# Performance work log

Hardware: AMD Instinct MI355X
Metric: run time of the kernel (lower is better)

The kernel has to match this reference:

```python
import jax, jax.numpy as jnp
import numpy as np

B, T, HID = 1, 2048, 2048
H = 16            # num_heads == num_key_value_heads
D = HID // H      # head_dim == feature_dim == 128
EPS = 1e-5


def _layer_norm(x, eps=1e-5):
    mu = jnp.mean(x, axis=-1, keepdims=True)
    var = jnp.mean((x - mu) ** 2, axis=-1, keepdims=True)
    return (x - mu) * jax.lax.rsqrt(var + eps)


def _feature_map(x, gamma, beta):
    # ReBased feature map, flatten=False (parallel mode): affine then LayerNorm
    return _layer_norm(x * gamma + beta)


def setup_inputs() -> dict:
    key = jax.random.key(0)
    ks = jax.random.split(key, 8)
    s = HID ** -0.5
    return {
        "hidden_states": jax.random.normal(ks[0], (B, T, HID), jnp.float32),
        "Wq": jax.random.normal(ks[1], (HID, HID), jnp.float32) * s,
        "Wk": jax.random.normal(ks[2], (HID, HID), jnp.float32) * s,
        "Wv": jax.random.normal(ks[3], (HID, HID), jnp.float32) * s,
        "Wo": jax.random.normal(ks[4], (HID, HID), jnp.float32) * s,
        "gamma": 1.0 + 0.1 * jax.random.normal(ks[5], (D,), jnp.float32),
        "beta": 0.1 * jax.random.normal(ks[6], (D,), jnp.float32),
    }


def reference(hidden_states, Wq, Wk, Wv, Wo, gamma, beta):
    b, t, _ = hidden_states.shape
    # projections (nn.Linear: x @ W.T), split into heads: [b, t, h, d]
    q = (hidden_states @ Wq.T).reshape(b, t, H, D)
    k = (hidden_states @ Wk.T).reshape(b, t, H, D)
    v = (hidden_states @ Wv.T).reshape(b, t, H, D)
    # ReBased feature map (no quadratic flatten in parallel mode)
    q = _feature_map(q, gamma, beta)
    k = _feature_map(k, gamma, beta)
    # parallel_rebased: scale q, quadratic score, causal mask, normalize
    q = q * (D ** -0.5)
    attn = jnp.einsum('bqhd,bkhd->bhqk', q, k) ** 2  # (q.k)^2
    mask = jnp.tril(jnp.ones((t, t), dtype=bool))
    attn = jnp.where(mask, attn, 0.0)
    o = jnp.einsum('bhqk,bkhd->bqhd', attn, v)       # [b, t, h, d]
    z = jnp.sum(attn, axis=-1)                       # [b, h, t]
    o = o / (jnp.swapaxes(z, 1, 2)[..., None] + EPS)
    o = o.reshape(b, t, H * D)
    return o @ Wo.T
```

## Files before the change

### kernel.cpp

```cpp
#include <hip/hip_runtime.h>
#include <hip/hip_bf16.h>
#include <stdint.h>

typedef __bf16 bf16;
typedef __bf16 v8bf __attribute__((ext_vector_type(8)));
typedef float  v4f  __attribute__((ext_vector_type(4)));

#define TSEQ   2048
#define HIDDIM 2048
#define NHEAD  16
#define HDIM   128

__device__ __forceinline__ void async16(void* lds, const void* g)
{
    __builtin_amdgcn_global_load_lds(
        (__attribute__((address_space(1))) void*)(uintptr_t)g,
        (__attribute__((address_space(3))) void*)(unsigned int)(uintptr_t)lds,
        16, 0, 0);
}

__global__ __launch_bounds__(256) void conv5(const float* __restrict__ s0, bf16* __restrict__ d0,
                                             const float* __restrict__ s1, bf16* __restrict__ d1,
                                             const float* __restrict__ s2, bf16* __restrict__ d2,
                                             const float* __restrict__ s3, bf16* __restrict__ d3,
                                             const float* __restrict__ s4, bf16* __restrict__ d4)
{
    const float* src; bf16* dst;
    switch (blockIdx.y) {
        case 0: src = s0; dst = d0; break;
        case 1: src = s1; dst = d1; break;
        case 2: src = s2; dst = d2; break;
        case 3: src = s3; dst = d3; break;
        default: src = s4; dst = d4; break;
    }
    const size_t i = ((size_t)blockIdx.x * 256 + threadIdx.x) * 8;
    const float4 a = *(const float4*)(src + i);
    const float4 b = *(const float4*)(src + i + 4);
    v8bf o;
    o[0] = (bf16)a.x; o[1] = (bf16)a.y; o[2] = (bf16)a.z; o[3] = (bf16)a.w;
    o[4] = (bf16)b.x; o[5] = (bf16)b.y; o[6] = (bf16)b.z; o[7] = (bf16)b.w;
    *(v8bf*)(dst + i) = o;
}

template <typename CT>
__device__ __forceinline__ void gemm_body(const bf16* __restrict__ A,
                                          const bf16* __restrict__ B,
                                          CT* __restrict__ C,
                                          int m0, int n0, int K, int ldc)
{
    __shared__ __attribute__((aligned(16))) bf16 sA[128*32];
    __shared__ __attribute__((aligned(16))) bf16 sB[128*32];
    const int tid  = threadIdx.x;
    const int lane = tid & 63;
    const int w    = tid >> 6;
    const int wm   = w >> 1, wn = w & 1;
    const int quad = lane >> 4, lr = lane & 15;
    const int srow = lane >> 2;
    const int scol = (lane & 3) * 8;

    const bf16* gA0 = A + (size_t)(m0 + w*32 + srow) * K + scol;
    const bf16* gB0 = B + (size_t)(n0 + w*32 + srow) * K + scol;
    bf16* lA0 = &sA[w*1024];
    bf16* lB0 = &sB[w*1024];

    v4f acc[4][4] = {};

    for (int kt = 0; kt < K; kt += 32) {
        __syncthreads();
        async16(lA0,       gA0 + kt);
        async16(lA0 + 512, gA0 + (size_t)16*K + kt);
        async16(lB0,       gB0 + kt);
        async16(lB0 + 512, gB0 + (size_t)16*K + kt);
        __syncthreads();
        v8bf a[4], b[4];
#pragma unroll
        for (int i = 0; i < 4; ++i)
            a[i] = *(const v8bf*)&sA[(wm*64 + i*16 + lr)*32 + quad*8];
#pragma unroll
        for (int j = 0; j < 4; ++j)
            b[j] = *(const v8bf*)&sB[(wn*64 + j*16 + lr)*32 + quad*8];
#pragma unroll
        for (int i = 0; i < 4; ++i)
#pragma unroll
            for (int j = 0; j < 4; ++j)
                acc[i][j] = __builtin_amdgcn_mfma_f32_16x16x32_bf16(a[i], b[j], acc[i][j], 0, 0, 0);
    }

#pragma unroll
    for (int i = 0; i < 4; ++i) {
        const int row_b = m0 + wm*64 + i*16 + quad*4;
#pragma unroll
        for (int j = 0; j < 4; ++j) {
            const int col = n0 + wn*64 + j*16 + lr;
#pragma unroll
            for (int r = 0; r < 4; ++r)
                C[(size_t)(row_b + r)*ldc + col] = (CT)acc[i][j][r];
        }
    }
}

__global__ __launch_bounds__(256) void gemm_qkv(const bf16* __restrict__ A,
    const bf16* __restrict__ Wq, const bf16* __restrict__ Wk, const bf16* __restrict__ Wv,
    bf16* __restrict__ qb, bf16* __restrict__ kb, bf16* __restrict__ vb)
{
    const int which = blockIdx.x >> 4;
    const int n0 = (blockIdx.x & 15) * 128;
    const int m0 = blockIdx.y * 128;
    const bf16* B = (which == 0) ? Wq : (which == 1) ? Wk : Wv;
    bf16* C = (which == 0) ? qb : (which == 1) ? kb : vb;
    gemm_body<bf16>(A, B, C, m0, n0, HIDDIM, HIDDIM);
}

__global__ __launch_bounds__(256) void gemm_out(const bf16* __restrict__ A,
    const bf16* __restrict__ B, float* __restrict__ C)
{
    __shared__ __attribute__((aligned(16))) bf16 sA[128*32];
    __shared__ __attribute__((aligned(16))) bf16 sB[64*32];
    const int m0 = blockIdx.y * 128, n0 = blockIdx.x * 64;
    const int K = HIDDIM, ldc = HIDDIM;
    const int tid  = threadIdx.x;
    const int lane = tid & 63;
    const int w    = tid >> 6;
    const int wm   = w >> 1, wn = w & 1;
    const int quad = lane >> 4, lr = lane & 15;
    const int srow = lane >> 2;
    const int scol = (lane & 3) * 8;

    const bf16* gA0 = A + (size_t)(m0 + w*32 + srow) * K + scol;
    const bf16* gB0 = B + (size_t)(n0 + w*16 + srow) * K + scol;
    bf16* lA0 = &sA[w*1024];
    bf16* lB0 = &sB[w*512];

    v4f acc[4][2] = {};

    for (int kt = 0; kt < K; kt += 32) {
        __syncthreads();
        async16(lA0,       gA0 + kt);
        async16(lA0 + 512, gA0 + (size_t)16*K + kt);
        async16(lB0,       gB0 + kt);
        __syncthreads();
        v8bf a[4], b[2];
#pragma unroll
        for (int i = 0; i < 4; ++i)
            a[i] = *(const v8bf*)&sA[(wm*64 + i*16 + lr)*32 + quad*8];
#pragma unroll
        for (int j = 0; j < 2; ++j)
            b[j] = *(const v8bf*)&sB[(wn*32 + j*16 + lr)*32 + quad*8];
#pragma unroll
        for (int i = 0; i < 4; ++i)
#pragma unroll
            for (int j = 0; j < 2; ++j)
                acc[i][j] = __builtin_amdgcn_mfma_f32_16x16x32_bf16(a[i], b[j], acc[i][j], 0, 0, 0);
    }

#pragma unroll
    for (int i = 0; i < 4; ++i) {
        const int row_b = m0 + wm*64 + i*16 + quad*4;
#pragma unroll
        for (int j = 0; j < 2; ++j) {
            const int col = n0 + wn*32 + j*16 + lr;
#pragma unroll
            for (int r = 0; r < 4; ++r)
                C[(size_t)(row_b + r)*ldc + col] = acc[i][j][r];
        }
    }
}

__global__ __launch_bounds__(256) void fmap(bf16* __restrict__ qb, bf16* __restrict__ kb,
                                            const float* __restrict__ gamma,
                                            const float* __restrict__ beta)
{
    const int rid  = blockIdx.x * 4 + (threadIdx.x >> 6);
    const int lane = threadIdx.x & 63;
    bf16* base = (rid < TSEQ*NHEAD) ? (qb + (size_t)rid * HDIM)
                                    : (kb + (size_t)(rid - TSEQ*NHEAD) * HDIM);
    const float scale = (rid < TSEQ*NHEAD) ? 0.08838834764831845f : 1.0f;

    const bf16 x0b = base[lane*2], x1b = base[lane*2+1];
    const float g0 = gamma[lane*2], g1 = gamma[lane*2+1];
    const float b0 = beta[lane*2],  b1 = beta[lane*2+1];
    float x0 = (float)x0b*g0 + b0;
    float x1 = (float)x1b*g1 + b1;
    float s  = x0 + x1;
    float sq = x0*x0 + x1*x1;
#pragma unroll
    for (int off = 1; off < 64; off <<= 1) { s += __shfl_xor(s, off); sq += __shfl_xor(sq, off); }
    const float mu   = s * (1.0f/128.0f);
    float var        = sq * (1.0f/128.0f) - mu*mu;
    var = fmaxf(var, 0.0f);
    const float rstd = rsqrtf(var + 1e-5f);
    base[lane*2]   = (bf16)((x0 - mu) * rstd * scale);
    base[lane*2+1] = (bf16)((x1 - mu) * rstd * scale);
}

__global__ __launch_bounds__(256) void transpose2048(const bf16* __restrict__ src,
                                                     bf16* __restrict__ dst)
{
    __shared__ __attribute__((aligned(16))) bf16 tile[64][72];
    const int t0 = blockIdx.y * 64, c0 = blockIdx.x * 64;
    const int tid = threadIdx.x;
    const int r = tid >> 3;
    const int c = (tid & 7) * 8;
#pragma unroll
    for (int p = 0; p < 2; ++p) {
        const int rr = r + p*32;
        *(v8bf*)&tile[rr][c] = *(const v8bf*)(src + (size_t)(t0+rr)*HIDDIM + c0 + c);
    }
    __syncthreads();
#pragma unroll
    for (int p = 0; p < 2; ++p) {
        const int orow = r + p*32;
        v8bf o;
#pragma unroll
        for (int i = 0; i < 8; ++i) o[i] = tile[c + i][orow];
        *(v8bf*)(dst + (size_t)(c0+orow)*HIDDIM + t0 + c) = o;
    }
}

__global__ __launch_bounds__(256) void attn(const bf16* __restrict__ qb,
                                            const bf16* __restrict__ kb,
                                            const bf16* __restrict__ vt,
                                            bf16* __restrict__ ob)
{
    __shared__ __attribute__((aligned(16))) bf16 sK[64*136];
    __shared__ __attribute__((aligned(16))) bf16 sV[128*72];
    __shared__ __attribute__((aligned(16))) bf16 sS[64*72];
    const int h    = blockIdx.y;
    const int tile = 31 - blockIdx.x;
    const int tid  = threadIdx.x, lane = tid & 63, w = tid >> 6;
    const int quad = lane >> 4, lr = lane & 15;

    v8bf qa[4];
    {
        const bf16* q0 = qb + (size_t)(tile*64 + w*16 + lr)*HIDDIM + h*HDIM + quad*8;
#pragma unroll
        for (int ks = 0; ks < 4; ++ks)
            qa[ks] = *(const v8bf*)(q0 + ks*32);
    }

    const int rK = tid >> 4, cK = (tid & 15) * 8;
    const int rV = tid >> 3, cV = (tid & 7) * 8;

    v8bf curK[4], curV[4], nxtK[4], nxtV[4];
#pragma unroll
    for (int p = 0; p < 4; ++p) {
        curK[p] = *(const v8bf*)(kb + (size_t)(rK + p*16)*HIDDIM + h*HDIM + cK);
        curV[p] = *(const v8bf*)(vt + (size_t)(h*HDIM + rV + p*32)*HIDDIM + cV);
    }

    v4f  o[8] = {};
    float z[4] = {};
    const int nch = tile + 1;

    for (int ch = 0; ch < nch; ++ch) {
        const int s0 = ch * 64;
        const bool diag = (ch == tile);
        __syncthreads();
#pragma unroll
        for (int p = 0; p < 4; ++p)
            *(v8bf*)&sK[(rK + p*16)*136 + cK] = curK[p];
#pragma unroll
        for (int p = 0; p < 4; ++p)
            *(v8bf*)&sV[(rV + p*32)*72 + cV] = curV[p];
        if (ch + 1 < nch) {
            const int s1 = s0 + 64;
#pragma unroll
            for (int p = 0; p < 4; ++p) {
                nxtK[p] = *(const v8bf*)(kb + (size_t)(s1 + rK + p*16)*HIDDIM + h*HDIM + cK);
                nxtV[p] = *(const v8bf*)(vt + (size_t)(h*HDIM + rV + p*32)*HIDDIM + s1 + cV);
            }
        }
        __syncthreads();

        v8bf kbf[4][4];
#pragma unroll
        for (int nj = 0; nj < 4; ++nj)
#pragma unroll
            for (int ks = 0; ks < 4; ++ks)
                kbf[nj][ks] = *(const v8bf*)&sK[(nj*16 + lr)*136 + ks*32 + quad*8];
        const int row_l = w*16 + quad*4;
        const int qg    = tile*64 + row_l;
#pragma unroll
        for (int nj = 0; nj < 4; ++nj) {
            v4f s4 = {0.f, 0.f, 0.f, 0.f};
#pragma unroll
            for (int ks = 0; ks < 4; ++ks)
                s4 = __builtin_amdgcn_mfma_f32_16x16x32_bf16(qa[ks], kbf[nj][ks], s4, 0, 0, 0);
            const int col = nj*16 + lr;
            const int sg  = s0 + col;
#pragma unroll
            for (int r = 0; r < 4; ++r) {
                float val = s4[r] * s4[r];
                if (diag && (sg > qg + r)) val = 0.0f;
                const bf16 vb16 = (bf16)val;
                z[r] += (float)vb16;
                sS[(row_l + r)*72 + col] = vb16;
            }
        }

#pragma unroll
        for (int ks = 0; ks < 2; ++ks) {
            const v8bf sa = *(const v8bf*)&sS[(w*16 + lr)*72 + ks*32 + quad*8];
#pragma unroll
            for (int nd = 0; nd < 8; ++nd) {
                const v8bf vbf = *(const v8bf*)&sV[(nd*16 + lr)*72 + ks*32 + quad*8];
                o[nd] = __builtin_amdgcn_mfma_f32_16x16x32_bf16(sa, vbf, o[nd], 0, 0, 0);
            }
        }

        if (ch + 1 < nch) {
#pragma unroll
            for (int p = 0; p < 4; ++p) { curK[p] = nxtK[p]; curV[p] = nxtV[p]; }
        }
    }

#pragma unroll
    for (int r = 0; r < 4; ++r) {
        float zz = z[r];
        zz += __shfl_xor(zz, 1); zz += __shfl_xor(zz, 2);
        zz += __shfl_xor(zz, 4); zz += __shfl_xor(zz, 8);
        z[r] = zz + 1e-5f;
    }

    {
        const int row_l = w*16 + quad*4;
        const size_t rbase = (size_t)(tile*64 + row_l)*HIDDIM + h*HDIM;
#pragma unroll
        for (int nd = 0; nd < 8; ++nd) {
            const int col = nd*16 + lr;
#pragma unroll
            for (int r = 0; r < 4; ++r)
                ob[rbase + (size_t)r*HIDDIM + col] = (bf16)(o[nd][r] / z[r]);
        }
    }
}

extern "C" void kernel_launch(void* const* d_in, const int* in_sizes, int n_in,
                              void* d_out, int out_size, void* d_ws, size_t ws_size,
                              hipStream_t stream)
{
    const float* hs    = (const float*)d_in[0];
    const float* Wq    = (const float*)d_in[1];
    const float* Wk    = (const float*)d_in[2];
    const float* Wv    = (const float*)d_in[3];
    const float* Wo    = (const float*)d_in[4];
    const float* gamma = (const float*)d_in[5];
    const float* beta  = (const float*)d_in[6];
    float* outp = (float*)d_out;

    const size_t MAT = (size_t)TSEQ * HIDDIM;

    bf16* ws   = (bf16*)d_ws;
    bf16* hs_b = ws + 0*MAT;
    bf16* vt   = hs_b;
    bf16* Wv_b = ws + 1*MAT;
    bf16* Wo_b = ws + 2*MAT;
    bf16* qb   = ws + 3*MAT;
    bf16* kb   = ws + 4*MAT;
    bf16* vb   = ws + 5*MAT;
    bf16* ob   = vb;
    bf16* Wq_b = (bf16*)d_out;
    bf16* Wk_b = (bf16*)d_out + MAT;

    conv5<<<dim3(2048, 5), 256, 0, stream>>>(hs, hs_b, Wq, Wq_b, Wk, Wk_b, Wv, Wv_b, Wo, Wo_b);
    gemm_qkv<<<dim3(48, 16), 256, 0, stream>>>(hs_b, Wq_b, Wk_b, Wv_b, qb, kb, vb);
    fmap<<<dim3(2*TSEQ*NHEAD/4), 256, 0, stream>>>(qb, kb, gamma, beta);
    transpose2048<<<dim3(32, 32), 256, 0, stream>>>(vb, vt);
    attn<<<dim3(32, 16), 256, 0, stream>>>(qb, kb, vt, ob);
    gemm_out<<<dim3(32, 16), 256, 0, stream>>>(ob, Wo_b, outp);
}
```

Before: 299.5 us.

## Pair causal tiles per block and split KV chunks across two wave groups

The attention kernel now launches 16x16 blocks of 512 threads. Each block handles two complementary query tiles (31-pr and pr) so the causal work per block is balanced. Within a block, two groups of four waves each process alternate 64-key chunks into separate LDS buffers, and the partial O and Z accumulators are reduced through shared memory at the end. This targets load imbalance from the causal triangle and the tail, at the cost of much more LDS per block (around 140KB, which limits occupancy) and an extra reduction step.

```diff
diff --git a/kernel.cpp b/kernel.cpp
--- a/kernel.cpp
+++ b/kernel.cpp
@@ -217,120 +217,156 @@
     }
 }
 
-__global__ __launch_bounds__(256) void attn(const bf16* __restrict__ qb,
-                                            const bf16* __restrict__ kb,
-                                            const bf16* __restrict__ vt,
-                                            bf16* __restrict__ ob)
-{
-    __shared__ __attribute__((aligned(16))) bf16 sK[64*136];
-    __shared__ __attribute__((aligned(16))) bf16 sV[128*72];
-    __shared__ __attribute__((aligned(16))) bf16 sS[64*72];
+__global__ __launch_bounds__(512, 2) void attn(const bf16* __restrict__ qb,
+                                               const bf16* __restrict__ kb,
+                                               const bf16* __restrict__ vt,
+                                               bf16* __restrict__ ob)
+{
+    __shared__ __attribute__((aligned(16))) bf16 sK[2*64*136];
+    __shared__ __attribute__((aligned(16))) bf16 sV[2*128*72];
+    __shared__ __attribute__((aligned(16))) bf16 sS[2*64*72];
+    __shared__ __attribute__((aligned(16))) float sO[64*129];
+    __shared__ __attribute__((aligned(16))) float sZ[64*17];
+
     const int h    = blockIdx.y;
-    const int tile = 31 - blockIdx.x;
-    const int tid  = threadIdx.x, lane = tid & 63, w = tid >> 6;
+    const int pr   = blockIdx.x;
+    const int tid  = threadIdx.x, lane = tid & 63;
+    const int w    = tid >> 6;
+    const int g    = w >> 2;
+    const int ww   = w & 3;
     const int quad = lane >> 4, lr = lane & 15;
-
-    v8bf qa[4];
-    {
-        const bf16* q0 = qb + (size_t)(tile*64 + w*16 + lr)*HIDDIM + h*HDIM + quad*8;
-#pragma unroll
-        for (int ks = 0; ks < 4; ++ks)
-            qa[ks] = *(const v8bf*)(q0 + ks*32);
-    }
-
-    const int rK = tid >> 4, cK = (tid & 15) * 8;
-    const int rV = tid >> 3, cV = (tid & 7) * 8;
-
-    v8bf curK[4], curV[4], nxtK[4], nxtV[4];
-#pragma unroll
-    for (int p = 0; p < 4; ++p) {
-        curK[p] = *(const v8bf*)(kb + (size_t)(rK + p*16)*HIDDIM + h*HDIM + cK);
-        curV[p] = *(const v8bf*)(vt + (size_t)(h*HDIM + rV + p*32)*HIDDIM + cV);
-    }
-
-    v4f  o[8] = {};
-    float z[4] = {};
-    const int nch = tile + 1;
-
-    for (int ch = 0; ch < nch; ++ch) {
-        const int s0 = ch * 64;
-        const bool diag = (ch == tile);
-        __syncthreads();
-#pragma unroll
-        for (int p = 0; p < 4; ++p)
-            *(v8bf*)&sK[(rK + p*16)*136 + cK] = curK[p];
-#pragma unroll
-        for (int p = 0; p < 4; ++p)
-            *(v8bf*)&sV[(rV + p*32)*72 + cV] = curV[p];
-        if (ch + 1 < nch) {
-            const int s1 = s0 + 64;
+    const int rs   = tid >> 4;
+    const int cs   = (tid & 15) * 8;
+
+#pragma unroll
+    for (int ti = 0; ti < 2; ++ti) {
+        const int tile = ti ? pr : (31 - pr);
+        const int nch  = tile + 1;
+
+        v8bf qa[4];
+        {
+            const bf16* q0 = qb + (size_t)(tile*64 + ww*16 + lr)*HIDDIM + h*HDIM + quad*8;
+#pragma unroll
+            for (int ks = 0; ks < 4; ++ks)
+                qa[ks] = *(const v8bf*)(q0 + ks*32);
+        }
+
+        v4f  o[8] = {};
+        float z[4] = {0.f, 0.f, 0.f, 0.f};
+
+        v8bf curK[4], curV[4], nxtK[4], nxtV[4];
+#pragma unroll
+        for (int p = 0; p < 4; ++p) {
+            curK[p] = *(const v8bf*)(kb + (size_t)(rs + p*32)*HIDDIM + h*HDIM + cs);
+            curV[p] = *(const v8bf*)(vt + (size_t)(h*HDIM + rs + p*32)*HIDDIM + cs);
+        }
+
+        for (int ich = 0; ich < nch; ich += 2) {
+            __syncthreads();
 #pragma unroll
             for (int p = 0; p < 4; ++p) {
-                nxtK[p] = *(const v8bf*)(kb + (size_t)(s1 + rK + p*16)*HIDDIM + h*HDIM + cK);
-                nxtV[p] = *(const v8bf*)(vt + (size_t)(h*HDIM + rV + p*32)*HIDDIM + s1 + cV);
-            }
-        }
-        __syncthreads();
-
-        v8bf kbf[4][4];
-#pragma unroll
-        for (int nj = 0; nj < 4; ++nj)
-#pragma unroll
-            for (int ks = 0; ks < 4; ++ks)
-                kbf[nj][ks] = *(const v8bf*)&sK[(nj*16 + lr)*136 + ks*32 + quad*8];
-        const int row_l = w*16 + quad*4;
-        const int qg    = tile*64 + row_l;
-#pragma unroll
-        for (int nj = 0; nj < 4; ++nj) {
-            v4f s4 = {0.f, 0.f, 0.f, 0.f};
-#pragma unroll
-            for (int ks = 0; ks < 4; ++ks)
-                s4 = __builtin_amdgcn_mfma_f32_16x16x32_bf16(qa[ks], kbf[nj][ks], s4, 0, 0, 0);
-            const int col = nj*16 + lr;
-            const int sg  = s0 + col;
+                const int r = rs + p*32;
+                *(v8bf*)&sK[(r>>6)*8704 + (r&63)*136 + cs] = curK[p];
+            }
+#pragma unroll
+            for (int p = 0; p < 4; ++p)
+                *(v8bf*)&sV[(cs>>6)*9216 + (rs + p*32)*72 + (cs & 63)] = curV[p];
+
+            if (ich + 2 < nch) {
+                const int s1 = (ich + 2) * 64;
+#pragma unroll
+                for (int p = 0; p < 4; ++p) {
+                    nxtK[p] = *(const v8bf*)(kb + (size_t)(s1 + rs + p*32)*HIDDIM + h*HDIM + cs);
+                    nxtV[p] = *(const v8bf*)(vt + (size_t)(h*HDIM + rs + p*32)*HIDDIM + s1 + cs);
+                }
+            }
+            __syncthreads();
+
+            const int ch = ich + g;
+            if (ch < nch) {
+                const bf16* sKg = &sK[g*8704];
+                const bf16* sVg = &sV[g*9216];
+                bf16*       sSg = &sS[g*4608];
+                const bool  diag = (ch == tile);
+                const int   s0   = ch * 64;
+
+                v8bf kbf[4][4];
+#pragma unroll
+                for (int nj = 0; nj < 4; ++nj)
+#pragma unroll
+                    for (int ks = 0; ks < 4; ++ks)
+                        kbf[nj][ks] = *(const v8bf*)&sKg[(nj*16 + lr)*136 + ks*32 + quad*8];
+                const int row_l = ww*16 + quad*4;
+                const int qg    = tile*64 + row_l;
+#pragma unroll
+                for (int nj = 0; nj < 4; ++nj) {
+                    v4f s4 = {0.f, 0.f, 0.f, 0.f};
+#pragma unroll
+                    for (int ks = 0; ks < 4; ++ks)
+                        s4 = __builtin_amdgcn_mfma_f32_16x16x32_bf16(qa[ks], kbf[nj][ks], s4, 0, 0, 0);
+                    const int col = nj*16 + lr;
+                    const int sg  = s0 + col;
+#pragma unroll
+                    for (int r = 0; r < 4; ++r) {
+                        float val = s4[r] * s4[r];
+                        if (diag && (sg > qg + r)) val = 0.0f;
+                        const bf16 vb16 = (bf16)val;
+                        z[r] += (float)vb16;
+                        sSg[(row_l + r)*72 + col] = vb16;
+                    }
+                }
+
+#pragma unroll
+                for (int ks = 0; ks < 2; ++ks) {
+                    const v8bf sa = *(const v8bf*)&sSg[(ww*16 + lr)*72 + ks*32 + quad*8];
+#pragma unroll
+                    for (int nd = 0; nd < 8; ++nd) {
+                        const v8bf vbf = *(const v8bf*)&sVg[(nd*16 + lr)*72 + ks*32 + quad*8];
+                        o[nd] = __builtin_amdgcn_mfma_f32_16x16x32_bf16(sa, vbf, o[nd], 0, 0, 0);
+                    }
+                }
+            }
+
+            if (ich + 2 < nch) {
+#pragma unroll
+                for (int p = 0; p < 4; ++p) { curK[p] = nxtK[p]; curV[p] = nxtV[p]; }
+            }
+        }
+
+        const int row_l = ww*16 + quad*4;
+        __syncthreads();
+        if (g == 1) {
+#pragma unroll
+            for (int nd = 0; nd < 8; ++nd)
+#pragma unroll
+                for (int r = 0; r < 4; ++r)
+                    sO[(row_l + r)*129 + nd*16 + lr] = o[nd][r];
+#pragma unroll
+            for (int r = 0; r < 4; ++r)
+                sZ[(row_l + r)*17 + lr] = z[r];
+        }
+        __syncthreads();
+        if (g == 0) {
+#pragma unroll
+            for (int nd = 0; nd < 8; ++nd)
+#pragma unroll
+                for (int r = 0; r < 4; ++r)
+                    o[nd][r] += sO[(row_l + r)*129 + nd*16 + lr];
 #pragma unroll
             for (int r = 0; r < 4; ++r) {
-                float val = s4[r] * s4[r];
-                if (diag && (sg > qg + r)) val = 0.0f;
-                const bf16 vb16 = (bf16)val;
-                z[r] += (float)vb16;
-                sS[(row_l + r)*72 + col] = vb16;
-            }
-        }
-
-#pragma unroll
-        for (int ks = 0; ks < 2; ++ks) {
-            const v8bf sa = *(const v8bf*)&sS[(w*16 + lr)*72 + ks*32 + quad*8];
+                float zz = z[r] + sZ[(row_l + r)*17 + lr];
+                zz += __shfl_xor(zz, 1); zz += __shfl_xor(zz, 2);
+                zz += __shfl_xor(zz, 4); zz += __shfl_xor(zz, 8);
+                z[r] = zz + 1e-5f;
+            }
+            const size_t rbase = (size_t)(tile*64 + row_l)*HIDDIM + h*HDIM;
 #pragma unroll
             for (int nd = 0; nd < 8; ++nd) {
-                const v8bf vbf = *(const v8bf*)&sV[(nd*16 + lr)*72 + ks*32 + quad*8];
-                o[nd] = __builtin_amdgcn_mfma_f32_16x16x32_bf16(sa, vbf, o[nd], 0, 0, 0);
-            }
-        }
-
-        if (ch + 1 < nch) {
-#pragma unroll
-            for (int p = 0; p < 4; ++p) { curK[p] = nxtK[p]; curV[p] = nxtV[p]; }
-        }
-    }
-
-#pragma unroll
-    for (int r = 0; r < 4; ++r) {
-        float zz = z[r];
-        zz += __shfl_xor(zz, 1); zz += __shfl_xor(zz, 2);
-        zz += __shfl_xor(zz, 4); zz += __shfl_xor(zz, 8);
-        z[r] = zz + 1e-5f;
-    }
-
-    {
-        const int row_l = w*16 + quad*4;
-        const size_t rbase = (size_t)(tile*64 + row_l)*HIDDIM + h*HDIM;
-#pragma unroll
-        for (int nd = 0; nd < 8; ++nd) {
-            const int col = nd*16 + lr;
-#pragma unroll
-            for (int r = 0; r < 4; ++r)
-                ob[rbase + (size_t)r*HIDDIM + col] = (bf16)(o[nd][r] / z[r]);
+                const int col = nd*16 + lr;
+#pragma unroll
+                for (int r = 0; r < 4; ++r)
+                    ob[rbase + (size_t)r*HIDDIM + col] = (bf16)(o[nd][r] / z[r]);
+            }
         }
     }
 }
@@ -366,6 +402,6 @@
     gemm_qkv<<<dim3(48, 16), 256, 0, stream>>>(hs_b, Wq_b, Wk_b, Wv_b, qb, kb, vb);
     fmap<<<dim3(2*TSEQ*NHEAD/4), 256, 0, stream>>>(qb, kb, gamma, beta);
     transpose2048<<<dim3(32, 32), 256, 0, stream>>>(vb, vt);
-    attn<<<dim3(32, 16), 256, 0, stream>>>(qb, kb, vt, ob);
+    attn<<<dim3(16, 16), 512, 0, stream>>>(qb, kb, vt, ob);
     gemm_out<<<dim3(32, 16), 256, 0, stream>>>(ob, Wo_b, outp);
 }
```

Result: faster. 281.6 us (-6.0%).
